# Performance work log

Measured on AMD Instinct MI355X. Metric: run time of the kernel, lower is better.

## Reference

```python
import jax, jax.numpy as jnp
import numpy as np

N, IN_DIM, LAT, K = 32768, 128, 64, 8192
BETA = 1.25


def _linear_params(key, d_in, d_out):
    kw, kb = jax.random.split(key)
    lim = 1.0 / np.sqrt(d_in)
    W = jax.random.uniform(kw, (d_out, d_in), minval=-lim, maxval=lim, dtype=jnp.float32)
    b = jax.random.uniform(kb, (d_out,), minval=-lim, maxval=lim, dtype=jnp.float32)
    return W, b


def setup_inputs() -> dict:
    key = jax.random.key(0)
    ks = jax.random.split(key, 9)
    x = jax.random.normal(ks[0], (N, IN_DIM), dtype=jnp.float32)
    # encoder: 128 -> 256 -> 128 -> 64
    enc_W1, enc_b1 = _linear_params(ks[1], IN_DIM, 256)
    enc_W2, enc_b2 = _linear_params(ks[2], 256, 128)
    enc_W3, enc_b3 = _linear_params(ks[3], 128, LAT)
    # codebook: uniform(-1/K, 1/K)
    emb = jax.random.uniform(ks[4], (K, LAT), minval=-1.0 / K, maxval=1.0 / K, dtype=jnp.float32)
    # decoder: 64 -> 128 -> 256 -> (mu: 128, log_var: 128)
    dec_W1, dec_b1 = _linear_params(ks[5], LAT, 128)
    dec_W2, dec_b2 = _linear_params(ks[6], 128, 256)
    dec_Wmu, dec_bmu = _linear_params(ks[7], 256, IN_DIM)
    dec_Wlv, dec_blv = _linear_params(ks[8], 256, IN_DIM)
    return {
        'x': x,
        'enc_W1': enc_W1, 'enc_b1': enc_b1,
        'enc_W2': enc_W2, 'enc_b2': enc_b2,
        'enc_W3': enc_W3, 'enc_b3': enc_b3,
        'emb': emb,
        'dec_W1': dec_W1, 'dec_b1': dec_b1,
        'dec_W2': dec_W2, 'dec_b2': dec_b2,
        'dec_Wmu': dec_Wmu, 'dec_bmu': dec_bmu,
        'dec_Wlv': dec_Wlv, 'dec_blv': dec_blv,
    }


def reference(x, enc_W1, enc_b1, enc_W2, enc_b2, enc_W3, enc_b3, emb,
              dec_W1, dec_b1, dec_W2, dec_b2, dec_Wmu, dec_bmu, dec_Wlv, dec_blv):
    sg = jax.lax.stop_gradient
    # encoder MLP
    h = jax.nn.relu(x @ enc_W1.T + enc_b1)
    h = jax.nn.relu(h @ enc_W2.T + enc_b2)
    lat = h @ enc_W3.T + enc_b3                      # [N, D]
    # vector quantizer: [N, K] pairwise squared distances
    d = (jnp.sum(lat * lat, axis=1, keepdims=True)
         + jnp.sum(emb * emb, axis=1)
         - 2.0 * lat @ emb.T)
    inds = jnp.argmin(d, axis=1)                     # [N]
    one_hot = jax.nn.one_hot(inds, K, dtype=jnp.float32)   # [N, K]
    q = emb[inds]                                    # gather == one_hot @ emb
    commitment = jnp.mean((sg(q) - lat) ** 2)
    embedding_loss = jnp.mean((q - sg(lat)) ** 2)
    vq_loss = BETA * commitment + embedding_loss
    z = lat + sg(q - lat)                            # straight-through
    # decoder MLP
    h = jax.nn.relu(z @ dec_W1.T + dec_b1)
    h = jax.nn.relu(h @ dec_W2.T + dec_b2)
    x_hat = h @ dec_Wmu.T + dec_bmu
    x_hat_var = h @ dec_Wlv.T + dec_blv
    return x_hat, x_hat_var, one_hot, vq_loss
```

## Files before the change

### kernel.cpp

```cpp
#include <hip/hip_runtime.h>
#include <cfloat>
#include <climits>

#define TPB 256


typedef float f32x4 __attribute__((ext_vector_type(4)));

__device__ __forceinline__ void nt_store4(float* p, float4 v) {
  f32x4 nv;
  nv.x = v.x; nv.y = v.y; nv.z = v.z; nv.w = v.w;
  __builtin_nontemporal_store(nv, reinterpret_cast<f32x4*>(p));
}

__global__ __launch_bounds__(TPB) void wt_kernel(
    const float* __restrict__ W1, const float* __restrict__ W2,
    const float* __restrict__ W3, const float* __restrict__ U1,
    const float* __restrict__ U2, const float* __restrict__ Umu,
    const float* __restrict__ Ulv, float* __restrict__ wt) {
  __shared__ float sB[64 * 68];
  const int b = blockIdx.x;
  const float* src; int R, C, lt; float* dst;
  if (b < 8)       { src = W1;  R = 256; C = 128; dst = wt;          lt = b; }
  else if (b < 16) { src = W2;  R = 128; C = 256; dst = wt + 32768;  lt = b - 8; }
  else if (b < 18) { src = W3;  R = 64;  C = 128; dst = wt + 65536;  lt = b - 16; }
  else if (b < 20) { src = U1;  R = 128; C = 64;  dst = wt + 73728;  lt = b - 18; }
  else if (b < 28) { src = U2;  R = 256; C = 128; dst = wt + 81920;  lt = b - 20; }
  else if (b < 36) { src = Umu; R = 128; C = 256; dst = wt + 114688; lt = b - 28; }
  else             { src = Ulv; R = 128; C = 256; dst = wt + 147456; lt = b - 36; }
  const int tiles_r = R >> 6;
  const int r0 = (lt % tiles_r) << 6, c0 = (lt / tiles_r) << 6;
  const int t = threadIdx.x;
  for (int v = t; v < 1024; v += TPB) {
    const int c4 = v & 15, r = v >> 4;
    const float4 w =
        *reinterpret_cast<const float4*>(src + (size_t)(r0 + r) * C + c0 + 4 * c4);
    *reinterpret_cast<float4*>(&sB[r * 68 + 4 * c4]) = w;
  }
  __syncthreads();
  for (int v = t; v < 1024; v += TPB) {
    const int r4 = v & 15, c = v >> 4;
    float4 o;
    o.x = sB[(4 * r4 + 0) * 68 + c];
    o.y = sB[(4 * r4 + 1) * 68 + c];
    o.z = sB[(4 * r4 + 2) * 68 + c];
    o.w = sB[(4 * r4 + 3) * 68 + c];
    *reinterpret_cast<float4*>(dst + (size_t)(c0 + c) * R + r0 + 4 * r4) = o;
  }
}

__global__ __launch_bounds__(TPB) void embt_kernel(const float* __restrict__ emb,
                                                   float* __restrict__ embT,
                                                   float* __restrict__ En) {
  __shared__ float sB[64 * 68];
  const int c0 = blockIdx.x * 64;
  const int t = threadIdx.x;
  for (int v = t; v < 1024; v += TPB) {
    const int d4 = v & 15, r = v >> 4;
    const float4 e =
        *reinterpret_cast<const float4*>(emb + (size_t)(c0 + r) * 64 + 4 * d4);
    *reinterpret_cast<float4*>(&sB[r * 68 + 4 * d4]) = e;
  }
  __syncthreads();
  if (t < 64) {
    const float* row = &sB[t * 68];
    float q[8];
#pragma unroll
    for (int j = 0; j < 8; ++j) q[j] = __fmul_rn(row[j], row[j]);
#pragma unroll
    for (int m = 1; m < 8; ++m)
#pragma unroll
      for (int j = 0; j < 8; ++j) {
        const float v = row[m * 8 + j];
        q[j] = __fadd_rn(q[j], __fmul_rn(v, v));
      }
    En[c0 + t] = __fadd_rn(
        __fadd_rn(__fadd_rn(q[0], q[1]), __fadd_rn(q[2], q[3])),
        __fadd_rn(__fadd_rn(q[4], q[5]), __fadd_rn(q[6], q[7])));
  }
  for (int v = t; v < 1024; v += TPB) {
    const int r4 = v & 15, d = v >> 4;
    float4 o;
    o.x = sB[(4 * r4 + 0) * 68 + d];
    o.y = sB[(4 * r4 + 1) * 68 + d];
    o.z = sB[(4 * r4 + 2) * 68 + d];
    o.w = sB[(4 * r4 + 3) * 68 + d];
    *reinterpret_cast<float4*>(embT + (size_t)d * 8192 + c0 + 4 * r4) = o;
  }
}

__global__ __launch_bounds__(512) void enc_fused(
    const float* __restrict__ x, const float* __restrict__ WT1,
    const float* __restrict__ WT2, const float* __restrict__ WT3,
    const float* __restrict__ b1, const float* __restrict__ b2,
    const float* __restrict__ b3, float* __restrict__ lat) {
  __shared__ float sX[128 * 68];
  __shared__ float sH1[256 * 68];
  __shared__ float sH2[128 * 68];
  const int t = threadIdx.x;
  const int m0 = blockIdx.x * 64;

  for (int v = t; v < 2048; v += 512) {
    const int k4 = v & 31, r = v >> 5;
    const float4 xv =
        *reinterpret_cast<const float4*>(x + (size_t)(m0 + r) * 128 + 4 * k4);
    float* dst = &sX[(4 * k4) * 68 + r];
    dst[0] = xv.x; dst[68] = xv.y; dst[136] = xv.z; dst[204] = xv.w;
  }
  __syncthreads();

  {
    const int cg8 = (t & 31) * 8, rg4 = (t >> 5) * 4;
    float acc[4][8] = {};
#pragma unroll 8
    for (int k = 0; k < 128; ++k) {
      const float4 a = *reinterpret_cast<const float4*>(&sX[k * 68 + rg4]);
      const float* wr = WT1 + (size_t)k * 256 + cg8;
      const float4 b0 = *reinterpret_cast<const float4*>(wr);
      const float4 b1v = *reinterpret_cast<const float4*>(wr + 4);
      const float av[4] = {a.x, a.y, a.z, a.w};
      const float bv[8] = {b0.x, b0.y, b0.z, b0.w, b1v.x, b1v.y, b1v.z, b1v.w};
#pragma unroll
      for (int i = 0; i < 4; ++i)
#pragma unroll
        for (int j = 0; j < 8; ++j) acc[i][j] = fmaf(av[i], bv[j], acc[i][j]);
    }
#pragma unroll
    for (int j = 0; j < 8; ++j) {
      const int col = cg8 + j;
      const float bj = b1[col];
#pragma unroll
      for (int i = 0; i < 4; ++i) {
        const float h = __fadd_rn(acc[i][j], bj);
        sH1[col * 68 + rg4 + i] = h > 0.f ? h : 0.f;
      }
    }
  }
  __syncthreads();

  {
    const int cg4 = (t & 31) * 4, rg4 = (t >> 5) * 4;
    float acc[4][4] = {};
#pragma unroll 8
    for (int k = 0; k < 256; ++k) {
      const float4 a = *reinterpret_cast<const float4*>(&sH1[k * 68 + rg4]);
      const float4 bb =
          *reinterpret_cast<const float4*>(WT2 + (size_t)k * 128 + cg4);
      const float av[4] = {a.x, a.y, a.z, a.w};
      const float bv[4] = {bb.x, bb.y, bb.z, bb.w};
#pragma unroll
      for (int i = 0; i < 4; ++i)
#pragma unroll
        for (int j = 0; j < 4; ++j) acc[i][j] = fmaf(av[i], bv[j], acc[i][j]);
    }
#pragma unroll
    for (int j = 0; j < 4; ++j) {
      const int col = cg4 + j;
      const float bj = b2[col];
#pragma unroll
      for (int i = 0; i < 4; ++i) {
        const float h = __fadd_rn(acc[i][j], bj);
        sH2[col * 68 + rg4 + i] = h > 0.f ? h : 0.f;
      }
    }
  }
  __syncthreads();

  {
    const int cg4 = (t & 15) * 4, rg2 = (t >> 4) * 2;
    float acc[2][4] = {};
#pragma unroll 8
    for (int k = 0; k < 128; ++k) {
      const float2 a = *reinterpret_cast<const float2*>(&sH2[k * 68 + rg2]);
      const float4 bb =
          *reinterpret_cast<const float4*>(WT3 + (size_t)k * 64 + cg4);
      const float av[2] = {a.x, a.y};
      const float bv[4] = {bb.x, bb.y, bb.z, bb.w};
#pragma unroll
      for (int i = 0; i < 2; ++i)
#pragma unroll
        for (int j = 0; j < 4; ++j) acc[i][j] = fmaf(av[i], bv[j], acc[i][j]);
    }
#pragma unroll
    for (int i = 0; i < 2; ++i) {
      float4 o;
      o.x = __fadd_rn(acc[i][0], b3[cg4 + 0]);
      o.y = __fadd_rn(acc[i][1], b3[cg4 + 1]);
      o.z = __fadd_rn(acc[i][2], b3[cg4 + 2]);
      o.w = __fadd_rn(acc[i][3], b3[cg4 + 3]);
      *reinterpret_cast<float4*>(lat + (size_t)(m0 + rg2 + i) * 64 + cg4) = o;
    }
  }
}

__global__ __launch_bounds__(512, 2) void vq_kernel(
    const float* __restrict__ lat, const float* __restrict__ embT,
    const float* __restrict__ En, int* __restrict__ inds,
    float* __restrict__ lossp, float* __restrict__ oh) {
  __shared__ float sL[64 * 132];
  __shared__ float sE[64 * 260];
  __shared__ float snl[128];
  __shared__ int ridx[128];
  __shared__ float lacc;
  const int t = threadIdx.x;
  const int cg = t & 31;
  const int rg = t >> 5;
  const int cg4 = cg * 4;
  const int rg4 = rg * 4;
  const int m0 = blockIdx.x * 128;

  for (int v = t; v < 2048; v += 512) {
    const int r = v >> 4, d4 = v & 15;
    const float4 lv =
        *reinterpret_cast<const float4*>(lat + (size_t)(m0 + r) * 64 + 4 * d4);
    float* dst = &sL[(4 * d4) * 132 + r];
    dst[0] = lv.x; dst[132] = lv.y; dst[264] = lv.z; dst[396] = lv.w;
  }
  for (int v = t; v < 4096; v += 512) {
    const int d = v >> 6, c4 = v & 63;
    *reinterpret_cast<float4*>(&sE[d * 260 + 4 * c4]) =
        *reinterpret_cast<const float4*>(embT + (size_t)d * 8192 + 4 * c4);
  }
  if (t == 0) lacc = 0.f;
  __syncthreads();
  if (t < 128) {
    float q[8];
#pragma unroll
    for (int j = 0; j < 8; ++j) {
      const float v = sL[j * 132 + t];
      q[j] = __fmul_rn(v, v);
    }
#pragma unroll
    for (int m = 1; m < 8; ++m)
#pragma unroll
      for (int j = 0; j < 8; ++j) {
        const float v = sL[(m * 8 + j) * 132 + t];
        q[j] = __fadd_rn(q[j], __fmul_rn(v, v));
      }
    snl[t] = __fadd_rn(
        __fadd_rn(__fadd_rn(q[0], q[1]), __fadd_rn(q[2], q[3])),
        __fadd_rn(__fadd_rn(q[4], q[5]), __fadd_rn(q[6], q[7])));
  }
  __syncthreads();
  float nl[8];
#pragma unroll
  for (int i = 0; i < 4; ++i) {
    nl[i] = snl[rg4 + i];
    nl[4 + i] = snl[64 + rg4 + i];
  }

  float v1[8];
  int i1[8];
#pragma unroll
  for (int i = 0; i < 8; ++i) { v1[i] = FLT_MAX; i1[i] = INT_MAX; }

  const float4 z = make_float4(0.f, 0.f, 0.f, 0.f);

  for (int ch = 0; ch < 32; ++ch) {
    const int c0 = ch << 8;
#pragma unroll
    for (int k = 0; k < 16; ++k) {
      const int v = t + (k << 9);
      const int r = v >> 6, c4 = v & 63;
      nt_store4(oh + (size_t)(m0 + r) * 8192 + c0 + 4 * c4, z);
    }
    float4 pf[8];
    if (ch < 31) {
      const int cn = c0 + 256;
#pragma unroll
      for (int k = 0; k < 8; ++k) {
        const int v = t + (k << 9);
        const int d = v >> 6, c4 = v & 63;
        pf[k] = *reinterpret_cast<const float4*>(embT + (size_t)d * 8192 +
                                                 cn + 4 * c4);
      }
    }
    const float4 EA = *reinterpret_cast<const float4*>(En + c0 + cg4);
    const float4 EB = *reinterpret_cast<const float4*>(En + c0 + 128 + cg4);

    float acc[8][8] = {};
#pragma unroll 2
    for (int d = 0; d < 64; ++d) {
      const float4 a0 = *reinterpret_cast<const float4*>(&sL[d * 132 + rg4]);
      const float4 a1 =
          *reinterpret_cast<const float4*>(&sL[d * 132 + 64 + rg4]);
      const float4 b0 = *reinterpret_cast<const float4*>(&sE[d * 260 + cg4]);
      const float4 b1 =
          *reinterpret_cast<const float4*>(&sE[d * 260 + 128 + cg4]);
      const float av[8] = {a0.x, a0.y, a0.z, a0.w, a1.x, a1.y, a1.z, a1.w};
      const float bv[8] = {b0.x, b0.y, b0.z, b0.w, b1.x, b1.y, b1.z, b1.w};
#pragma unroll
      for (int i = 0; i < 8; ++i)
#pragma unroll
        for (int j = 0; j < 8; ++j) acc[i][j] = fmaf(av[i], bv[j], acc[i][j]);
    }
    const float Ev[8] = {EA.x, EA.y, EA.z, EA.w, EB.x, EB.y, EB.z, EB.w};
#pragma unroll
    for (int j = 0; j < 8; ++j) {
      const int c = c0 + (j < 4 ? cg4 + j : 128 + cg4 + (j - 4));
      const float Ec = Ev[j];
#pragma unroll
      for (int i = 0; i < 8; ++i) {
        const float t1 = __fadd_rn(nl[i], Ec);
        const float s = __fsub_rn(t1, __fmul_rn(2.0f, acc[i][j]));
        if (s < v1[i]) { v1[i] = s; i1[i] = c; }
      }
    }
    __syncthreads();
    if (ch < 31) {
#pragma unroll
      for (int k = 0; k < 8; ++k) {
        const int v = t + (k << 9);
        const int d = v >> 6, c4 = v & 63;
        *reinterpret_cast<float4*>(&sE[d * 260 + 4 * c4]) = pf[k];
      }
    }
    __syncthreads();
  }

#pragma unroll
  for (int m = 16; m >= 1; m >>= 1) {
#pragma unroll
    for (int i = 0; i < 8; ++i) {
      const float ov = __shfl_xor(v1[i], m);
      const int oi = __shfl_xor(i1[i], m);
      if (ov < v1[i] || (ov == v1[i] && oi < i1[i])) {
        v1[i] = ov; i1[i] = oi;
      }
    }
  }
  if (cg == 0) {
    float ls = 0.f;
#pragma unroll
    for (int i = 0; i < 4; ++i) {
      ridx[rg4 + i] = i1[i];
      inds[m0 + rg4 + i] = i1[i];
      ls += v1[i];
      ridx[64 + rg4 + i] = i1[4 + i];
      inds[m0 + 64 + rg4 + i] = i1[4 + i];
      ls += v1[4 + i];
    }
    atomicAdd(&lacc, ls);
  }
  __syncthreads();
  if (t == 0) lossp[blockIdx.x] = lacc;

#pragma unroll
  for (int k = 0; k < 16; ++k) {
    const int v = t + (k << 9);
    const int r = v >> 6, c4 = v & 63;
    const int ind = ridx[r];
    const int g4 = ind >> 2;
    if ((g4 & 63) == c4) {
      float4 o = make_float4(0.f, 0.f, 0.f, 0.f);
      reinterpret_cast<float*>(&o)[ind & 3] = 1.f;
      nt_store4(oh + (size_t)(m0 + r) * 8192 + 4 * g4, o);
    }
  }
}

__global__ __launch_bounds__(512) void dec_fused(
    const float* __restrict__ emb, const int* __restrict__ inds,
    const float* __restrict__ WT1, const float* __restrict__ b1,
    const float* __restrict__ WT2, const float* __restrict__ b2,
    const float* __restrict__ WTmu, const float* __restrict__ bmu,
    const float* __restrict__ WTlv, const float* __restrict__ blv,
    float* __restrict__ xh, float* __restrict__ xv) {
  __shared__ float sQ[64 * 68];
  __shared__ float sG1[128 * 68];
  __shared__ float sG2[256 * 68];
  const int t = threadIdx.x;
  const int m0 = blockIdx.x * 64;

  for (int v = t; v < 1024; v += 512) {
    const int k4 = v & 15, r = v >> 4;
    const int id = inds[m0 + r];
    const float4 e =
        *reinterpret_cast<const float4*>(emb + (size_t)id * 64 + 4 * k4);
    float* dst = &sQ[(4 * k4) * 68 + r];
    dst[0] = e.x; dst[68] = e.y; dst[136] = e.z; dst[204] = e.w;
  }
  __syncthreads();

  {
    const int cg4 = (t & 31) * 4, rg4 = (t >> 5) * 4;
    float acc[4][4] = {};
#pragma unroll 8
    for (int k = 0; k < 64; ++k) {
      const float4 a = *reinterpret_cast<const float4*>(&sQ[k * 68 + rg4]);
      const float4 bb =
          *reinterpret_cast<const float4*>(WT1 + (size_t)k * 128 + cg4);
      const float av[4] = {a.x, a.y, a.z, a.w};
      const float bv[4] = {bb.x, bb.y, bb.z, bb.w};
#pragma unroll
      for (int i = 0; i < 4; ++i)
#pragma unroll
        for (int j = 0; j < 4; ++j) acc[i][j] = fmaf(av[i], bv[j], acc[i][j]);
    }
#pragma unroll
    for (int j = 0; j < 4; ++j) {
      const int col = cg4 + j;
      const float bj = b1[col];
#pragma unroll
      for (int i = 0; i < 4; ++i) {
        const float h = acc[i][j] + bj;
        sG1[col * 68 + rg4 + i] = h > 0.f ? h : 0.f;
      }
    }
  }
  __syncthreads();

  {
    const int cg8 = (t & 31) * 8, rg4 = (t >> 5) * 4;
    float acc[4][8] = {};
#pragma unroll 8
    for (int k = 0; k < 128; ++k) {
      const float4 a = *reinterpret_cast<const float4*>(&sG1[k * 68 + rg4]);
      const float* wr = WT2 + (size_t)k * 256 + cg8;
      const float4 b0 = *reinterpret_cast<const float4*>(wr);
      const float4 b1v = *reinterpret_cast<const float4*>(wr + 4);
      const float av[4] = {a.x, a.y, a.z, a.w};
      const float bv[8] = {b0.x, b0.y, b0.z, b0.w, b1v.x, b1v.y, b1v.z, b1v.w};
#pragma unroll
      for (int i = 0; i < 4; ++i)
#pragma unroll
        for (int j = 0; j < 8; ++j) acc[i][j] = fmaf(av[i], bv[j], acc[i][j]);
    }
#pragma unroll
    for (int j = 0; j < 8; ++j) {
      const int col = cg8 + j;
      const float bj = b2[col];
#pragma unroll
      for (int i = 0; i < 4; ++i) {
        const float h = acc[i][j] + bj;
        sG2[col * 68 + rg4 + i] = h > 0.f ? h : 0.f;
      }
    }
  }
  __syncthreads();

  for (int head = 0; head < 2; ++head) {
    const float* WT = head ? WTlv : WTmu;
    const float* bb_ = head ? blv : bmu;
    float* o = head ? xv : xh;
    const int cg4 = (t & 31) * 4, rg4 = (t >> 5) * 4;
    float acc[4][4] = {};
#pragma unroll 8
    for (int k = 0; k < 256; ++k) {
      const float4 a = *reinterpret_cast<const float4*>(&sG2[k * 68 + rg4]);
      const float4 bb =
          *reinterpret_cast<const float4*>(WT + (size_t)k * 128 + cg4);
      const float av[4] = {a.x, a.y, a.z, a.w};
      const float bv[4] = {bb.x, bb.y, bb.z, bb.w};
#pragma unroll
      for (int i = 0; i < 4; ++i)
#pragma unroll
        for (int j = 0; j < 4; ++j) acc[i][j] = fmaf(av[i], bv[j], acc[i][j]);
    }
#pragma unroll
    for (int i = 0; i < 4; ++i) {
      float4 ov;
      ov.x = acc[i][0] + bb_[cg4 + 0];
      ov.y = acc[i][1] + bb_[cg4 + 1];
      ov.z = acc[i][2] + bb_[cg4 + 2];
      ov.w = acc[i][3] + bb_[cg4 + 3];
      nt_store4(o + (size_t)(m0 + rg4 + i) * 128 + cg4, ov);
    }
  }
}

__global__ void fin_kernel(const float* __restrict__ lossp,
                           float* __restrict__ outp) {
  const int t = threadIdx.x;
  double s = 0.0;
  for (int i = t; i < 256; i += 64) s += (double)lossp[i];
#pragma unroll
  for (int m = 32; m >= 1; m >>= 1) s += __shfl_xor(s, m);
  if (t == 0) *outp = (float)(2.25 * s / (32768.0 * 64.0));
}

extern "C" void kernel_launch(void* const* d_in, const int* in_sizes, int n_in,
                              void* d_out, int out_size, void* d_ws,
                              size_t ws_size, hipStream_t stream) {
  const float* x = (const float*)d_in[0];
  const float* eW1 = (const float*)d_in[1];
  const float* eb1 = (const float*)d_in[2];
  const float* eW2 = (const float*)d_in[3];
  const float* eb2 = (const float*)d_in[4];
  const float* eW3 = (const float*)d_in[5];
  const float* eb3 = (const float*)d_in[6];
  const float* emb = (const float*)d_in[7];
  const float* dW1 = (const float*)d_in[8];
  const float* db1 = (const float*)d_in[9];
  const float* dW2 = (const float*)d_in[10];
  const float* db2 = (const float*)d_in[11];
  const float* dWmu = (const float*)d_in[12];
  const float* dbmu = (const float*)d_in[13];
  const float* dWlv = (const float*)d_in[14];
  const float* dblv = (const float*)d_in[15];

  float* out = (float*)d_out;
  float* xhat = out;
  float* xvar = out + 4194304;
  float* oh = out + 8388608;
  float* lossout = out + 276824064;

  float* lat = (float*)d_ws;
  float* En = lat + 2097152;
  float* lossp = En + 8192;
  int* inds = (int*)(lossp + 512);
  float* embT = (float*)(inds + 32768);
  float* wt = embT + 524288;
  float* wt1 = wt;
  float* wt2 = wt + 32768;
  float* wt3 = wt + 65536;
  float* uwt1 = wt + 73728;
  float* uwt2 = wt + 81920;
  float* uwtmu = wt + 114688;
  float* uwtlv = wt + 147456;

  wt_kernel<<<44, TPB, 0, stream>>>(eW1, eW2, eW3, dW1, dW2, dWmu, dWlv, wt);
  embt_kernel<<<128, TPB, 0, stream>>>(emb, embT, En);
  enc_fused<<<512, 512, 0, stream>>>(x, wt1, wt2, wt3, eb1, eb2, eb3, lat);
  vq_kernel<<<256, 512, 0, stream>>>(lat, embT, En, inds, lossp, oh);
  dec_fused<<<512, 512, 0, stream>>>(emb, inds, uwt1, db1, uwt2, db2, uwtmu,
                                     dbmu, uwtlv, dblv, xhat, xvar);
  fin_kernel<<<1, 64, 0, stream>>>(lossp, lossout);
}
```

Measured before the change: 782.2 us.

## Fuse encoder, VQ argmin and decoder into one per-tile mega kernel

Merges the encoder MLP, codebook nearest-neighbour search with one-hot writes, and decoder MLP into a single kernel that handles 64 rows per block. Latents and chosen indices stay in shared memory, so the lat and inds global round trips and two kernel launches go away. The VQ tile changes from 128 rows by 256 codes to 64 rows by 512 codes, with the codebook staged in two 32-dim halves and double-buffered through registers. In exchange, each codebook chunk is read and reused across only 64 rows instead of 128, so embT traffic doubles. Occupancy may also drop because of the large shared footprint and heavy register use.

```diff
diff --git a/kernel.cpp b/kernel.cpp
--- a/kernel.cpp
+++ b/kernel.cpp
@@ -89,382 +89,406 @@
   }
 }
 
-__global__ __launch_bounds__(512) void enc_fused(
+__global__ __launch_bounds__(512, 2) void mega_kernel(
     const float* __restrict__ x, const float* __restrict__ WT1,
     const float* __restrict__ WT2, const float* __restrict__ WT3,
     const float* __restrict__ b1, const float* __restrict__ b2,
-    const float* __restrict__ b3, float* __restrict__ lat) {
-  __shared__ float sX[128 * 68];
-  __shared__ float sH1[256 * 68];
-  __shared__ float sH2[128 * 68];
+    const float* __restrict__ b3, const float* __restrict__ embT,
+    const float* __restrict__ En, const float* __restrict__ emb,
+    const float* __restrict__ UT1, const float* __restrict__ ub1,
+    const float* __restrict__ UT2, const float* __restrict__ ub2,
+    const float* __restrict__ UTmu, const float* __restrict__ ubmu,
+    const float* __restrict__ UTlv, const float* __restrict__ ublv,
+    float* __restrict__ oh, float* __restrict__ xh, float* __restrict__ xv,
+    float* __restrict__ lossp) {
+  __shared__ float smem[34816];
+  __shared__ float sL[64 * 68];
+  __shared__ float snl[64];
+  __shared__ int ridx[64];
+  __shared__ float lacc;
   const int t = threadIdx.x;
   const int m0 = blockIdx.x * 64;
 
-  for (int v = t; v < 2048; v += 512) {
-    const int k4 = v & 31, r = v >> 5;
-    const float4 xv =
-        *reinterpret_cast<const float4*>(x + (size_t)(m0 + r) * 128 + 4 * k4);
-    float* dst = &sX[(4 * k4) * 68 + r];
-    dst[0] = xv.x; dst[68] = xv.y; dst[136] = xv.z; dst[204] = xv.w;
-  }
-  __syncthreads();
-
   {
-    const int cg8 = (t & 31) * 8, rg4 = (t >> 5) * 4;
-    float acc[4][8] = {};
+    float* const sX = smem;
+    float* const sH1 = smem + 8704;
+    float* const sH2 = smem + 26112;
+
+    for (int v = t; v < 2048; v += 512) {
+      const int k4 = v & 31, r = v >> 5;
+      const float4 xv =
+          *reinterpret_cast<const float4*>(x + (size_t)(m0 + r) * 128 + 4 * k4);
+      float* dst = &sX[(4 * k4) * 68 + r];
+      dst[0] = xv.x; dst[68] = xv.y; dst[136] = xv.z; dst[204] = xv.w;
+    }
+    __syncthreads();
+
+    {
+      const int cg8 = (t & 31) * 8, rg4 = (t >> 5) * 4;
+      float acc[4][8] = {};
 #pragma unroll 8
-    for (int k = 0; k < 128; ++k) {
-      const float4 a = *reinterpret_cast<const float4*>(&sX[k * 68 + rg4]);
-      const float* wr = WT1 + (size_t)k * 256 + cg8;
-      const float4 b0 = *reinterpret_cast<const float4*>(wr);
-      const float4 b1v = *reinterpret_cast<const float4*>(wr + 4);
-      const float av[4] = {a.x, a.y, a.z, a.w};
-      const float bv[8] = {b0.x, b0.y, b0.z, b0.w, b1v.x, b1v.y, b1v.z, b1v.w};
-#pragma unroll
-      for (int i = 0; i < 4; ++i)
-#pragma unroll
-        for (int j = 0; j < 8; ++j) acc[i][j] = fmaf(av[i], bv[j], acc[i][j]);
-    }
-#pragma unroll
-    for (int j = 0; j < 8; ++j) {
-      const int col = cg8 + j;
-      const float bj = b1[col];
-#pragma unroll
-      for (int i = 0; i < 4; ++i) {
-        const float h = __fadd_rn(acc[i][j], bj);
-        sH1[col * 68 + rg4 + i] = h > 0.f ? h : 0.f;
-      }
-    }
-  }
-  __syncthreads();
-
-  {
-    const int cg4 = (t & 31) * 4, rg4 = (t >> 5) * 4;
-    float acc[4][4] = {};
+      for (int k = 0; k < 128; ++k) {
+        const float4 a = *reinterpret_cast<const float4*>(&sX[k * 68 + rg4]);
+        const float* wr = WT1 + (size_t)k * 256 + cg8;
+        const float4 b0 = *reinterpret_cast<const float4*>(wr);
+        const float4 b1v = *reinterpret_cast<const float4*>(wr + 4);
+        const float av[4] = {a.x, a.y, a.z, a.w};
+        const float bv[8] = {b0.x, b0.y, b0.z, b0.w, b1v.x, b1v.y, b1v.z, b1v.w};
+#pragma unroll
+        for (int i = 0; i < 4; ++i)
+#pragma unroll
+          for (int j = 0; j < 8; ++j) acc[i][j] = fmaf(av[i], bv[j], acc[i][j]);
+      }
+#pragma unroll
+      for (int j = 0; j < 8; ++j) {
+        const int col = cg8 + j;
+        const float bj = b1[col];
+#pragma unroll
+        for (int i = 0; i < 4; ++i) {
+          const float h = __fadd_rn(acc[i][j], bj);
+          sH1[col * 68 + rg4 + i] = h > 0.f ? h : 0.f;
+        }
+      }
+    }
+    __syncthreads();
+
+    {
+      const int cg4 = (t & 31) * 4, rg4 = (t >> 5) * 4;
+      float acc[4][4] = {};
 #pragma unroll 8
-    for (int k = 0; k < 256; ++k) {
-      const float4 a = *reinterpret_cast<const float4*>(&sH1[k * 68 + rg4]);
-      const float4 bb =
-          *reinterpret_cast<const float4*>(WT2 + (size_t)k * 128 + cg4);
-      const float av[4] = {a.x, a.y, a.z, a.w};
-      const float bv[4] = {bb.x, bb.y, bb.z, bb.w};
-#pragma unroll
-      for (int i = 0; i < 4; ++i)
-#pragma unroll
-        for (int j = 0; j < 4; ++j) acc[i][j] = fmaf(av[i], bv[j], acc[i][j]);
-    }
-#pragma unroll
-    for (int j = 0; j < 4; ++j) {
-      const int col = cg4 + j;
-      const float bj = b2[col];
-#pragma unroll
-      for (int i = 0; i < 4; ++i) {
-        const float h = __fadd_rn(acc[i][j], bj);
-        sH2[col * 68 + rg4 + i] = h > 0.f ? h : 0.f;
-      }
-    }
-  }
-  __syncthreads();
-
-  {
-    const int cg4 = (t & 15) * 4, rg2 = (t >> 4) * 2;
-    float acc[2][4] = {};
+      for (int k = 0; k < 256; ++k) {
+        const float4 a = *reinterpret_cast<const float4*>(&sH1[k * 68 + rg4]);
+        const float4 bb =
+            *reinterpret_cast<const float4*>(WT2 + (size_t)k * 128 + cg4);
+        const float av[4] = {a.x, a.y, a.z, a.w};
+        const float bv[4] = {bb.x, bb.y, bb.z, bb.w};
+#pragma unroll
+        for (int i = 0; i < 4; ++i)
+#pragma unroll
+          for (int j = 0; j < 4; ++j) acc[i][j] = fmaf(av[i], bv[j], acc[i][j]);
+      }
+#pragma unroll
+      for (int j = 0; j < 4; ++j) {
+        const int col = cg4 + j;
+        const float bj = b2[col];
+#pragma unroll
+        for (int i = 0; i < 4; ++i) {
+          const float h = __fadd_rn(acc[i][j], bj);
+          sH2[col * 68 + rg4 + i] = h > 0.f ? h : 0.f;
+        }
+      }
+    }
+    __syncthreads();
+
+    {
+      const int cg4 = (t & 15) * 4, rg2 = (t >> 4) * 2;
+      float acc[2][4] = {};
 #pragma unroll 8
-    for (int k = 0; k < 128; ++k) {
-      const float2 a = *reinterpret_cast<const float2*>(&sH2[k * 68 + rg2]);
-      const float4 bb =
-          *reinterpret_cast<const float4*>(WT3 + (size_t)k * 64 + cg4);
-      const float av[2] = {a.x, a.y};
-      const float bv[4] = {bb.x, bb.y, bb.z, bb.w};
-#pragma unroll
-      for (int i = 0; i < 2; ++i)
-#pragma unroll
-        for (int j = 0; j < 4; ++j) acc[i][j] = fmaf(av[i], bv[j], acc[i][j]);
-    }
-#pragma unroll
-    for (int i = 0; i < 2; ++i) {
-      float4 o;
-      o.x = __fadd_rn(acc[i][0], b3[cg4 + 0]);
-      o.y = __fadd_rn(acc[i][1], b3[cg4 + 1]);
-      o.z = __fadd_rn(acc[i][2], b3[cg4 + 2]);
-      o.w = __fadd_rn(acc[i][3], b3[cg4 + 3]);
-      *reinterpret_cast<float4*>(lat + (size_t)(m0 + rg2 + i) * 64 + cg4) = o;
-    }
-  }
-}
-
-__global__ __launch_bounds__(512, 2) void vq_kernel(
-    const float* __restrict__ lat, const float* __restrict__ embT,
-    const float* __restrict__ En, int* __restrict__ inds,
-    float* __restrict__ lossp, float* __restrict__ oh) {
-  __shared__ float sL[64 * 132];
-  __shared__ float sE[64 * 260];
-  __shared__ float snl[128];
-  __shared__ int ridx[128];
-  __shared__ float lacc;
-  const int t = threadIdx.x;
-  const int cg = t & 31;
-  const int rg = t >> 5;
-  const int cg4 = cg * 4;
-  const int rg4 = rg * 4;
-  const int m0 = blockIdx.x * 128;
-
-  for (int v = t; v < 2048; v += 512) {
-    const int r = v >> 4, d4 = v & 15;
-    const float4 lv =
-        *reinterpret_cast<const float4*>(lat + (size_t)(m0 + r) * 64 + 4 * d4);
-    float* dst = &sL[(4 * d4) * 132 + r];
-    dst[0] = lv.x; dst[132] = lv.y; dst[264] = lv.z; dst[396] = lv.w;
-  }
-  for (int v = t; v < 4096; v += 512) {
-    const int d = v >> 6, c4 = v & 63;
-    *reinterpret_cast<float4*>(&sE[d * 260 + 4 * c4]) =
-        *reinterpret_cast<const float4*>(embT + (size_t)d * 8192 + 4 * c4);
+      for (int k = 0; k < 128; ++k) {
+        const float2 a = *reinterpret_cast<const float2*>(&sH2[k * 68 + rg2]);
+        const float4 bb =
+            *reinterpret_cast<const float4*>(WT3 + (size_t)k * 64 + cg4);
+        const float av[2] = {a.x, a.y};
+        const float bv[4] = {bb.x, bb.y, bb.z, bb.w};
+#pragma unroll
+        for (int i = 0; i < 2; ++i)
+#pragma unroll
+          for (int j = 0; j < 4; ++j) acc[i][j] = fmaf(av[i], bv[j], acc[i][j]);
+      }
+#pragma unroll
+      for (int i = 0; i < 2; ++i) {
+        sL[(cg4 + 0) * 68 + rg2 + i] = __fadd_rn(acc[i][0], b3[cg4 + 0]);
+        sL[(cg4 + 1) * 68 + rg2 + i] = __fadd_rn(acc[i][1], b3[cg4 + 1]);
+        sL[(cg4 + 2) * 68 + rg2 + i] = __fadd_rn(acc[i][2], b3[cg4 + 2]);
+        sL[(cg4 + 3) * 68 + rg2 + i] = __fadd_rn(acc[i][3], b3[cg4 + 3]);
+      }
+    }
   }
   if (t == 0) lacc = 0.f;
   __syncthreads();
-  if (t < 128) {
-    float q[8];
-#pragma unroll
-    for (int j = 0; j < 8; ++j) {
-      const float v = sL[j * 132 + t];
-      q[j] = __fmul_rn(v, v);
-    }
-#pragma unroll
-    for (int m = 1; m < 8; ++m)
+
+  {
+    float* const sE = smem + 8704;
+    const int cg = t & 63;
+    const int rg = t >> 6;
+    const int cg4 = cg * 4;
+    const int rg8 = rg * 8;
+
+    if (t < 64) {
+      float q[8];
 #pragma unroll
       for (int j = 0; j < 8; ++j) {
-        const float v = sL[(m * 8 + j) * 132 + t];
-        q[j] = __fadd_rn(q[j], __fmul_rn(v, v));
-      }
-    snl[t] = __fadd_rn(
-        __fadd_rn(__fadd_rn(q[0], q[1]), __fadd_rn(q[2], q[3])),
-        __fadd_rn(__fadd_rn(q[4], q[5]), __fadd_rn(q[6], q[7])));
-  }
-  __syncthreads();
-  float nl[8];
-#pragma unroll
-  for (int i = 0; i < 4; ++i) {
-    nl[i] = snl[rg4 + i];
-    nl[4 + i] = snl[64 + rg4 + i];
-  }
-
-  float v1[8];
-  int i1[8];
-#pragma unroll
-  for (int i = 0; i < 8; ++i) { v1[i] = FLT_MAX; i1[i] = INT_MAX; }
-
-  const float4 z = make_float4(0.f, 0.f, 0.f, 0.f);
-
-  for (int ch = 0; ch < 32; ++ch) {
-    const int c0 = ch << 8;
+        const float v = sL[j * 68 + t];
+        q[j] = __fmul_rn(v, v);
+      }
+#pragma unroll
+      for (int m = 1; m < 8; ++m)
+#pragma unroll
+        for (int j = 0; j < 8; ++j) {
+          const float v = sL[(m * 8 + j) * 68 + t];
+          q[j] = __fadd_rn(q[j], __fmul_rn(v, v));
+        }
+      snl[t] = __fadd_rn(
+          __fadd_rn(__fadd_rn(q[0], q[1]), __fadd_rn(q[2], q[3])),
+          __fadd_rn(__fadd_rn(q[4], q[5]), __fadd_rn(q[6], q[7])));
+    }
+#pragma unroll
+    for (int k = 0; k < 8; ++k) {
+      const int v = t + (k << 9);
+      const int dr = v >> 7, c4 = v & 127;
+      *reinterpret_cast<float4*>(&sE[dr * 516 + 4 * c4]) =
+          *reinterpret_cast<const float4*>(embT + (size_t)dr * 8192 + 4 * c4);
+    }
+    __syncthreads();
+
+    float nl[8];
+#pragma unroll
+    for (int i = 0; i < 8; ++i) nl[i] = snl[rg8 + i];
+
+    float v1[8];
+    int i1[8];
+#pragma unroll
+    for (int i = 0; i < 8; ++i) { v1[i] = FLT_MAX; i1[i] = INT_MAX; }
+
+    const float4 z = make_float4(0.f, 0.f, 0.f, 0.f);
+
+    for (int ch = 0; ch < 16; ++ch) {
+      const int c0 = ch << 9;
+      float acc[8][8] = {};
+      float4 EA, EB;
+      float4 pf[8];
+
+#pragma unroll
+      for (int k = 0; k < 8; ++k) {
+        const int v = t + (k << 9);
+        const int r = v >> 7, c4 = v & 127;
+        nt_store4(oh + (size_t)(m0 + r) * 8192 + c0 + 4 * c4, z);
+      }
+      EA = *reinterpret_cast<const float4*>(En + c0 + cg4);
+      EB = *reinterpret_cast<const float4*>(En + c0 + 256 + cg4);
+#pragma unroll
+      for (int k = 0; k < 8; ++k) {
+        const int v = t + (k << 9);
+        const int dr = v >> 7, c4 = v & 127;
+        pf[k] = *reinterpret_cast<const float4*>(
+            embT + (size_t)(32 + dr) * 8192 + c0 + 4 * c4);
+      }
+#pragma unroll 2
+      for (int d = 0; d < 32; ++d) {
+        const float4 a0 = *reinterpret_cast<const float4*>(&sL[d * 68 + rg8]);
+        const float4 a1 =
+            *reinterpret_cast<const float4*>(&sL[d * 68 + rg8 + 4]);
+        const float4 b0 = *reinterpret_cast<const float4*>(&sE[d * 516 + cg4]);
+        const float4 b1 =
+            *reinterpret_cast<const float4*>(&sE[d * 516 + 256 + cg4]);
+        const float av[8] = {a0.x, a0.y, a0.z, a0.w, a1.x, a1.y, a1.z, a1.w};
+        const float bv[8] = {b0.x, b0.y, b0.z, b0.w, b1.x, b1.y, b1.z, b1.w};
+#pragma unroll
+        for (int i = 0; i < 8; ++i)
+#pragma unroll
+          for (int j = 0; j < 8; ++j) acc[i][j] = fmaf(av[i], bv[j], acc[i][j]);
+      }
+      __syncthreads();
+#pragma unroll
+      for (int k = 0; k < 8; ++k) {
+        const int v = t + (k << 9);
+        const int dr = v >> 7, c4 = v & 127;
+        *reinterpret_cast<float4*>(&sE[dr * 516 + 4 * c4]) = pf[k];
+      }
+      __syncthreads();
+
+#pragma unroll
+      for (int k = 8; k < 16; ++k) {
+        const int v = t + (k << 9);
+        const int r = v >> 7, c4 = v & 127;
+        nt_store4(oh + (size_t)(m0 + r) * 8192 + c0 + 4 * c4, z);
+      }
+      if (ch < 15) {
+#pragma unroll
+        for (int k = 0; k < 8; ++k) {
+          const int v = t + (k << 9);
+          const int dr = v >> 7, c4 = v & 127;
+          pf[k] = *reinterpret_cast<const float4*>(
+              embT + (size_t)dr * 8192 + c0 + 512 + 4 * c4);
+        }
+      }
+#pragma unroll 2
+      for (int d = 0; d < 32; ++d) {
+        const int dd = 32 + d;
+        const float4 a0 = *reinterpret_cast<const float4*>(&sL[dd * 68 + rg8]);
+        const float4 a1 =
+            *reinterpret_cast<const float4*>(&sL[dd * 68 + rg8 + 4]);
+        const float4 b0 = *reinterpret_cast<const float4*>(&sE[d * 516 + cg4]);
+        const float4 b1 =
+            *reinterpret_cast<const float4*>(&sE[d * 516 + 256 + cg4]);
+        const float av[8] = {a0.x, a0.y, a0.z, a0.w, a1.x, a1.y, a1.z, a1.w};
+        const float bv[8] = {b0.x, b0.y, b0.z, b0.w, b1.x, b1.y, b1.z, b1.w};
+#pragma unroll
+        for (int i = 0; i < 8; ++i)
+#pragma unroll
+          for (int j = 0; j < 8; ++j) acc[i][j] = fmaf(av[i], bv[j], acc[i][j]);
+      }
+      const float Ev[8] = {EA.x, EA.y, EA.z, EA.w, EB.x, EB.y, EB.z, EB.w};
+#pragma unroll
+      for (int j = 0; j < 8; ++j) {
+        const int c = c0 + (j < 4 ? cg4 + j : 256 + cg4 + (j - 4));
+        const float Ec = Ev[j];
+#pragma unroll
+        for (int i = 0; i < 8; ++i) {
+          const float t1 = __fadd_rn(nl[i], Ec);
+          const float s = __fsub_rn(t1, __fmul_rn(2.0f, acc[i][j]));
+          if (s < v1[i]) { v1[i] = s; i1[i] = c; }
+        }
+      }
+      __syncthreads();
+      if (ch < 15) {
+#pragma unroll
+        for (int k = 0; k < 8; ++k) {
+          const int v = t + (k << 9);
+          const int dr = v >> 7, c4 = v & 127;
+          *reinterpret_cast<float4*>(&sE[dr * 516 + 4 * c4]) = pf[k];
+        }
+      }
+      __syncthreads();
+    }
+
+#pragma unroll
+    for (int m = 32; m >= 1; m >>= 1) {
+#pragma unroll
+      for (int i = 0; i < 8; ++i) {
+        const float ov = __shfl_xor(v1[i], m);
+        const int oi = __shfl_xor(i1[i], m);
+        if (ov < v1[i] || (ov == v1[i] && oi < i1[i])) {
+          v1[i] = ov; i1[i] = oi;
+        }
+      }
+    }
+    if (cg == 0) {
+      float ls = 0.f;
+#pragma unroll
+      for (int i = 0; i < 8; ++i) {
+        ridx[rg8 + i] = i1[i];
+        ls += v1[i];
+      }
+      atomicAdd(&lacc, ls);
+    }
+    __syncthreads();
+    if (t == 0) lossp[blockIdx.x] = lacc;
+
 #pragma unroll
     for (int k = 0; k < 16; ++k) {
       const int v = t + (k << 9);
-      const int r = v >> 6, c4 = v & 63;
-      nt_store4(oh + (size_t)(m0 + r) * 8192 + c0 + 4 * c4, z);
-    }
-    float4 pf[8];
-    if (ch < 31) {
-      const int cn = c0 + 256;
-#pragma unroll
-      for (int k = 0; k < 8; ++k) {
-        const int v = t + (k << 9);
-        const int d = v >> 6, c4 = v & 63;
-        pf[k] = *reinterpret_cast<const float4*>(embT + (size_t)d * 8192 +
-                                                 cn + 4 * c4);
-      }
-    }
-    const float4 EA = *reinterpret_cast<const float4*>(En + c0 + cg4);
-    const float4 EB = *reinterpret_cast<const float4*>(En + c0 + 128 + cg4);
-
-    float acc[8][8] = {};
-#pragma unroll 2
-    for (int d = 0; d < 64; ++d) {
-      const float4 a0 = *reinterpret_cast<const float4*>(&sL[d * 132 + rg4]);
-      const float4 a1 =
-          *reinterpret_cast<const float4*>(&sL[d * 132 + 64 + rg4]);
-      const float4 b0 = *reinterpret_cast<const float4*>(&sE[d * 260 + cg4]);
-      const float4 b1 =
-          *reinterpret_cast<const float4*>(&sE[d * 260 + 128 + cg4]);
-      const float av[8] = {a0.x, a0.y, a0.z, a0.w, a1.x, a1.y, a1.z, a1.w};
-      const float bv[8] = {b0.x, b0.y, b0.z, b0.w, b1.x, b1.y, b1.z, b1.w};
-#pragma unroll
-      for (int i = 0; i < 8; ++i)
-#pragma unroll
-        for (int j = 0; j < 8; ++j) acc[i][j] = fmaf(av[i], bv[j], acc[i][j]);
-    }
-    const float Ev[8] = {EA.x, EA.y, EA.z, EA.w, EB.x, EB.y, EB.z, EB.w};
-#pragma unroll
-    for (int j = 0; j < 8; ++j) {
-      const int c = c0 + (j < 4 ? cg4 + j : 128 + cg4 + (j - 4));
-      const float Ec = Ev[j];
-#pragma unroll
-      for (int i = 0; i < 8; ++i) {
-        const float t1 = __fadd_rn(nl[i], Ec);
-        const float s = __fsub_rn(t1, __fmul_rn(2.0f, acc[i][j]));
-        if (s < v1[i]) { v1[i] = s; i1[i] = c; }
-      }
-    }
-    __syncthreads();
-    if (ch < 31) {
-#pragma unroll
-      for (int k = 0; k < 8; ++k) {
-        const int v = t + (k << 9);
-        const int d = v >> 6, c4 = v & 63;
-        *reinterpret_cast<float4*>(&sE[d * 260 + 4 * c4]) = pf[k];
-      }
-    }
-    __syncthreads();
-  }
-
-#pragma unroll
-  for (int m = 16; m >= 1; m >>= 1) {
-#pragma unroll
-    for (int i = 0; i < 8; ++i) {
-      const float ov = __shfl_xor(v1[i], m);
-      const int oi = __shfl_xor(i1[i], m);
-      if (ov < v1[i] || (ov == v1[i] && oi < i1[i])) {
-        v1[i] = ov; i1[i] = oi;
-      }
-    }
-  }
-  if (cg == 0) {
-    float ls = 0.f;
-#pragma unroll
-    for (int i = 0; i < 4; ++i) {
-      ridx[rg4 + i] = i1[i];
-      inds[m0 + rg4 + i] = i1[i];
-      ls += v1[i];
-      ridx[64 + rg4 + i] = i1[4 + i];
-      inds[m0 + 64 + rg4 + i] = i1[4 + i];
-      ls += v1[4 + i];
-    }
-    atomicAdd(&lacc, ls);
+      const int r = v >> 7, c4 = v & 127;
+      const int ind = ridx[r];
+      const int g4 = ind >> 2;
+      if ((g4 & 127) == c4) {
+        float4 o = make_float4(0.f, 0.f, 0.f, 0.f);
+        reinterpret_cast<float*>(&o)[ind & 3] = 1.f;
+        nt_store4(oh + (size_t)(m0 + r) * 8192 + 4 * g4, o);
+      }
+    }
   }
   __syncthreads();
-  if (t == 0) lossp[blockIdx.x] = lacc;
-
-#pragma unroll
-  for (int k = 0; k < 16; ++k) {
-    const int v = t + (k << 9);
-    const int r = v >> 6, c4 = v & 63;
-    const int ind = ridx[r];
-    const int g4 = ind >> 2;
-    if ((g4 & 63) == c4) {
-      float4 o = make_float4(0.f, 0.f, 0.f, 0.f);
-      reinterpret_cast<float*>(&o)[ind & 3] = 1.f;
-      nt_store4(oh + (size_t)(m0 + r) * 8192 + 4 * g4, o);
-    }
-  }
-}
-
-__global__ __launch_bounds__(512) void dec_fused(
-    const float* __restrict__ emb, const int* __restrict__ inds,
-    const float* __restrict__ WT1, const float* __restrict__ b1,
-    const float* __restrict__ WT2, const float* __restrict__ b2,
-    const float* __restrict__ WTmu, const float* __restrict__ bmu,
-    const float* __restrict__ WTlv, const float* __restrict__ blv,
-    float* __restrict__ xh, float* __restrict__ xv) {
-  __shared__ float sQ[64 * 68];
-  __shared__ float sG1[128 * 68];
-  __shared__ float sG2[256 * 68];
-  const int t = threadIdx.x;
-  const int m0 = blockIdx.x * 64;
-
-  for (int v = t; v < 1024; v += 512) {
-    const int k4 = v & 15, r = v >> 4;
-    const int id = inds[m0 + r];
-    const float4 e =
-        *reinterpret_cast<const float4*>(emb + (size_t)id * 64 + 4 * k4);
-    float* dst = &sQ[(4 * k4) * 68 + r];
-    dst[0] = e.x; dst[68] = e.y; dst[136] = e.z; dst[204] = e.w;
-  }
-  __syncthreads();
 
   {
-    const int cg4 = (t & 31) * 4, rg4 = (t >> 5) * 4;
-    float acc[4][4] = {};
+    float* const sQ = smem;
+    float* const sG1 = smem + 4352;
+    float* const sG2 = smem + 13056;
+
+    for (int v = t; v < 1024; v += 512) {
+      const int k4 = v & 15, r = v >> 4;
+      const int id = ridx[r];
+      const float4 e =
+          *reinterpret_cast<const float4*>(emb + (size_t)id * 64 + 4 * k4);
+      float* dst = &sQ[(4 * k4) * 68 + r];
+      dst[0] = e.x; dst[68] = e.y; dst[136] = e.z; dst[204] = e.w;
+    }
+    __syncthreads();
+
+    {
+      const int cg4 = (t & 31) * 4, rg4 = (t >> 5) * 4;
+      float acc[4][4] = {};
 #pragma unroll 8
-    for (int k = 0; k < 64; ++k) {
-      const float4 a = *reinterpret_cast<const float4*>(&sQ[k * 68 + rg4]);
-      const float4 bb =
-          *reinterpret_cast<const float4*>(WT1 + (size_t)k * 128 + cg4);
-      const float av[4] = {a.x, a.y, a.z, a.w};
-      const float bv[4] = {bb.x, bb.y, bb.z, bb.w};
-#pragma unroll
-      for (int i = 0; i < 4; ++i)
-#pragma unroll
-        for (int j = 0; j < 4; ++j) acc[i][j] = fmaf(av[i], bv[j], acc[i][j]);
-    }
-#pragma unroll
-    for (int j = 0; j < 4; ++j) {
-      const int col = cg4 + j;
-      const float bj = b1[col];
+      for (int k = 0; k < 64; ++k) {
+        const float4 a = *reinterpret_cast<const float4*>(&sQ[k * 68 + rg4]);
+        const float4 bb =
+            *reinterpret_cast<const float4*>(UT1 + (size_t)k * 128 + cg4);
+        const float av[4] = {a.x, a.y, a.z, a.w};
+        const float bv[4] = {bb.x, bb.y, bb.z, bb.w};
+#pragma unroll
+        for (int i = 0; i < 4; ++i)
+#pragma unroll
+          for (int j = 0; j < 4; ++j) acc[i][j] = fmaf(av[i], bv[j], acc[i][j]);
+      }
+#pragma unroll
+      for (int j = 0; j < 4; ++j) {
+        const int col = cg4 + j;
+        const float bj = ub1[col];
+#pragma unroll
+        for (int i = 0; i < 4; ++i) {
+          const float h = acc[i][j] + bj;
+          sG1[col * 68 + rg4 + i] = h > 0.f ? h : 0.f;
+        }
+      }
+    }
+    __syncthreads();
+
+    {
+      const int cg8 = (t & 31) * 8, rg4 = (t >> 5) * 4;
+      float acc[4][8] = {};
+#pragma unroll 8
+      for (int k = 0; k < 128; ++k) {
+        const float4 a = *reinterpret_cast<const float4*>(&sG1[k * 68 + rg4]);
+        const float* wr = UT2 + (size_t)k * 256 + cg8;
+        const float4 b0 = *reinterpret_cast<const float4*>(wr);
+        const float4 b1v = *reinterpret_cast<const float4*>(wr + 4);
+        const float av[4] = {a.x, a.y, a.z, a.w};
+        const float bv[8] = {b0.x, b0.y, b0.z, b0.w, b1v.x, b1v.y, b1v.z, b1v.w};
+#pragma unroll
+        for (int i = 0; i < 4; ++i)
+#pragma unroll
+          for (int j = 0; j < 8; ++j) acc[i][j] = fmaf(av[i], bv[j], acc[i][j]);
+      }
+#pragma unroll
+      for (int j = 0; j < 8; ++j) {
+        const int col = cg8 + j;
+        const float bj = ub2[col];
+#pragma unroll
+        for (int i = 0; i < 4; ++i) {
+          const float h = acc[i][j] + bj;
+          sG2[col * 68 + rg4 + i] = h > 0.f ? h : 0.f;
+        }
+      }
+    }
+    __syncthreads();
+
+    for (int head = 0; head < 2; ++head) {
+      const float* WT = head ? UTlv : UTmu;
+      const float* bb_ = head ? ublv : ubmu;
+      float* o = head ? xv : xh;
+      const int cg4 = (t & 31) * 4, rg4 = (t >> 5) * 4;
+      float acc[4][4] = {};
+#pragma unroll 8
+      for (int k = 0; k < 256; ++k) {
+        const float4 a = *reinterpret_cast<const float4*>(&sG2[k * 68 + rg4]);
+        const float4 bb =
+            *reinterpret_cast<const float4*>(WT + (size_t)k * 128 + cg4);
+        const float av[4] = {a.x, a.y, a.z, a.w};
+        const float bv[4] = {bb.x, bb.y, bb.z, bb.w};
+#pragma unroll
+        for (int i = 0; i < 4; ++i)
+#pragma unroll
+          for (int j = 0; j < 4; ++j) acc[i][j] = fmaf(av[i], bv[j], acc[i][j]);
+      }
 #pragma unroll
       for (int i = 0; i < 4; ++i) {
-        const float h = acc[i][j] + bj;
-        sG1[col * 68 + rg4 + i] = h > 0.f ? h : 0.f;
-      }
-    }
-  }
-  __syncthreads();
-
-  {
-    const int cg8 = (t & 31) * 8, rg4 = (t >> 5) * 4;
-    float acc[4][8] = {};
-#pragma unroll 8
-    for (int k = 0; k < 128; ++k) {
-      const float4 a = *reinterpret_cast<const float4*>(&sG1[k * 68 + rg4]);
-      const float* wr = WT2 + (size_t)k * 256 + cg8;
-      const float4 b0 = *reinterpret_cast<const float4*>(wr);
-      const float4 b1v = *reinterpret_cast<const float4*>(wr + 4);
-      const float av[4] = {a.x, a.y, a.z, a.w};
-      const float bv[8] = {b0.x, b0.y, b0.z, b0.w, b1v.x, b1v.y, b1v.z, b1v.w};
-#pragma unroll
-      for (int i = 0; i < 4; ++i)
-#pragma unroll
-        for (int j = 0; j < 8; ++j) acc[i][j] = fmaf(av[i], bv[j], acc[i][j]);
-    }
-#pragma unroll
-    for (int j = 0; j < 8; ++j) {
-      const int col = cg8 + j;
-      const float bj = b2[col];
-#pragma unroll
-      for (int i = 0; i < 4; ++i) {
-        const float h = acc[i][j] + bj;
-        sG2[col * 68 + rg4 + i] = h > 0.f ? h : 0.f;
-      }
-    }
-  }
-  __syncthreads();
-
-  for (int head = 0; head < 2; ++head) {
-    const float* WT = head ? WTlv : WTmu;
-    const float* bb_ = head ? blv : bmu;
-    float* o = head ? xv : xh;
-    const int cg4 = (t & 31) * 4, rg4 = (t >> 5) * 4;
-    float acc[4][4] = {};
-#pragma unroll 8
-    for (int k = 0; k < 256; ++k) {
-      const float4 a = *reinterpret_cast<const float4*>(&sG2[k * 68 + rg4]);
-      const float4 bb =
-          *reinterpret_cast<const float4*>(WT + (size_t)k * 128 + cg4);
-      const float av[4] = {a.x, a.y, a.z, a.w};
-      const float bv[4] = {bb.x, bb.y, bb.z, bb.w};
-#pragma unroll
-      for (int i = 0; i < 4; ++i)
-#pragma unroll
-        for (int j = 0; j < 4; ++j) acc[i][j] = fmaf(av[i], bv[j], acc[i][j]);
-    }
-#pragma unroll
-    for (int i = 0; i < 4; ++i) {
-      float4 ov;
-      ov.x = acc[i][0] + bb_[cg4 + 0];
-      ov.y = acc[i][1] + bb_[cg4 + 1];
-      ov.z = acc[i][2] + bb_[cg4 + 2];
-      ov.w = acc[i][3] + bb_[cg4 + 3];
-      nt_store4(o + (size_t)(m0 + rg4 + i) * 128 + cg4, ov);
+        float4 ov;
+        ov.x = acc[i][0] + bb_[cg4 + 0];
+        ov.y = acc[i][1] + bb_[cg4 + 1];
+        ov.z = acc[i][2] + bb_[cg4 + 2];
+        ov.w = acc[i][3] + bb_[cg4 + 3];
+        nt_store4(o + (size_t)(m0 + rg4 + i) * 128 + cg4, ov);
+      }
     }
   }
 }
@@ -473,7 +497,7 @@
                            float* __restrict__ outp) {
   const int t = threadIdx.x;
   double s = 0.0;
-  for (int i = t; i < 256; i += 64) s += (double)lossp[i];
+  for (int i = t; i < 512; i += 64) s += (double)lossp[i];
 #pragma unroll
   for (int m = 32; m >= 1; m >>= 1) s += __shfl_xor(s, m);
   if (t == 0) *outp = (float)(2.25 * s / (32768.0 * 64.0));
@@ -521,9 +545,8 @@
 
   wt_kernel<<<44, TPB, 0, stream>>>(eW1, eW2, eW3, dW1, dW2, dWmu, dWlv, wt);
   embt_kernel<<<128, TPB, 0, stream>>>(emb, embT, En);
-  enc_fused<<<512, 512, 0, stream>>>(x, wt1, wt2, wt3, eb1, eb2, eb3, lat);
-  vq_kernel<<<256, 512, 0, stream>>>(lat, embT, En, inds, lossp, oh);
-  dec_fused<<<512, 512, 0, stream>>>(emb, inds, uwt1, db1, uwt2, db2, uwtmu,
-                                     dbmu, uwtlv, dblv, xhat, xvar);
+  mega_kernel<<<512, 512, 0, stream>>>(
+      x, wt1, wt2, wt3, eb1, eb2, eb3, embT, En, emb, uwt1, db1, uwt2, db2,
+      uwtmu, dbmu, uwtlv, dblv, oh, xhat, xvar, lossp);
   fin_kernel<<<1, 64, 0, stream>>>(lossp, lossout);
 }
```

After: 856.8 us. +9.5%, slower.
